# Performance work log

Measured on AMD Instinct MI355X. Metric: run time of the kernel, lower is better.

Reference implementation:

```python
import jax, jax.numpy as jnp
import numpy as np

NUM_CLASSES = 100
QUEUE_SIZE = 256
FEATURE_DIM = 1024
BATCH = 4096
EPS = 1e-12  # torch F.normalize eps


def _l2norm(x):
    n = jnp.linalg.norm(x, axis=-1, keepdims=True)
    return x / jnp.maximum(n, EPS)


def setup_inputs() -> dict:
    key = jax.random.key(0)
    k1, k2, k3, k4 = jax.random.split(key, 4)
    embeddings = jax.random.normal(k1, (BATCH, FEATURE_DIM), dtype=jnp.float32)
    labels = jax.random.randint(k2, (BATCH,), 0, NUM_CLASSES, dtype=jnp.int64)
    # buffer initialized as randn then L2-normalized (as in __init__)
    queue = _l2norm(jax.random.normal(k3, (NUM_CLASSES, QUEUE_SIZE, FEATURE_DIM), dtype=jnp.float32))
    queue_ptr = jax.random.randint(k4, (NUM_CLASSES,), 0, QUEUE_SIZE, dtype=jnp.int64)
    return {"embeddings": embeddings, "labels": labels, "queue": queue, "queue_ptr": queue_ptr}


def reference(embeddings, labels, queue, queue_ptr):
    # MemoryBank.update with tail_classes=None: store_idx == label.
    # Serial FIFO semantics: the k-th occurrence of class c in the batch is
    # written at slot (queue_ptr[c] + k) % queue_size.
    queue_size = queue.shape[1]
    emb = _l2norm(embeddings.astype(jnp.float32))  # (B, d)
    # rank[b] = number of earlier batch elements with the same label
    same = labels[:, None] == labels[None, :]           # (B, B)
    rank = jnp.sum(jnp.tril(same, k=-1), axis=1)        # (B,)
    slots = (queue_ptr[labels] + rank) % queue_size      # (B,)
    new_queue = queue.at[labels, slots].set(emb)
    return new_queue
```

## Files before the change

### kernel.cpp

```cpp
#include <hip/hip_runtime.h>

#define NUM_CLASSES 100
#define QUEUE_SIZE  256
#define FEATURE_DIM 1024
#define BATCH       4096
#define TOTAL_ROWS  (NUM_CLASSES * QUEUE_SIZE)
#define EPS         1e-12f

typedef float f32x4 __attribute__((ext_vector_type(4)));

__global__ __launch_bounds__(256) void compute_slots_kernel(
    const int* __restrict__ labels,
    const int* __restrict__ queue_ptr,
    int* __restrict__ inv)
{
    __shared__ int hist[NUM_CLASSES];
    __shared__ int s_lab[256];

    const int tid = threadIdx.x;
    const int chunk_start = blockIdx.x * 256;

    for (int i = tid; i < NUM_CLASSES; i += 256) hist[i] = 0;
    __syncthreads();

    for (int j = tid; j < chunk_start; j += 256) {
        atomicAdd(&hist[labels[j]], 1);
    }
    s_lab[tid] = labels[chunk_start + tid];
    __syncthreads();

    const int lab = s_lab[tid];
    int rank = hist[lab];
    for (int j = 0; j < tid; ++j) {
        rank += (s_lab[j] == lab) ? 1 : 0;
    }
    const int slot = (queue_ptr[lab] + rank) & (QUEUE_SIZE - 1);
    const int row  = lab * QUEUE_SIZE + slot;
    const int b    = chunk_start + tid;
    atomicMax(&inv[row], b);
}

__global__ __launch_bounds__(256) void fused_write_kernel(
    const float* __restrict__ queue,
    const float* __restrict__ emb,
    const int* __restrict__ inv,
    float* __restrict__ out)
{
    const int row = blockIdx.x;
    const int tid = threadIdx.x;
    const long base = (long)row * FEATURE_DIM;

    const int b = inv[row];

    if (b < 0) {
        const f32x4* src = reinterpret_cast<const f32x4*>(queue + base);
        f32x4*       dst = reinterpret_cast<f32x4*>(out + base);
        f32x4 v = __builtin_nontemporal_load(&src[tid]);
        __builtin_nontemporal_store(v, &dst[tid]);
        return;
    }

    const f32x4* src = reinterpret_cast<const f32x4*>(emb + (long)b * FEATURE_DIM);
    f32x4 v = src[tid];

    float ss = v.x * v.x + v.y * v.y + v.z * v.z + v.w * v.w;
    #pragma unroll
    for (int off = 32; off > 0; off >>= 1) {
        ss += __shfl_down(ss, off, 64);
    }

    __shared__ float s_part[4];
    const int lane = tid & 63;
    const int wave = tid >> 6;
    if (lane == 0) s_part[wave] = ss;
    __syncthreads();

    const float total = s_part[0] + s_part[1] + s_part[2] + s_part[3];
    const float inv_n = 1.0f / fmaxf(sqrtf(total), EPS);

    f32x4 o = v * inv_n;

    f32x4* dst = reinterpret_cast<f32x4*>(out + base);
    __builtin_nontemporal_store(o, &dst[tid]);
}

extern "C" void kernel_launch(void* const* d_in, const int* in_sizes, int n_in,
                              void* d_out, int out_size, void* d_ws, size_t ws_size,
                              hipStream_t stream)
{
    const float* embeddings = (const float*)d_in[0];
    const int*   labels     = (const int*)d_in[1];
    const float* queue      = (const float*)d_in[2];
    const int*   queue_ptr  = (const int*)d_in[3];

    float* out = (float*)d_out;
    int*   inv = (int*)d_ws;

    (void)hipMemsetAsync(inv, 0xFF, TOTAL_ROWS * sizeof(int), stream);

    compute_slots_kernel<<<BATCH / 256, 256, 0, stream>>>(labels, queue_ptr, inv);

    fused_write_kernel<<<TOTAL_ROWS, 256, 0, stream>>>(queue, embeddings, inv, out);
}
```

Measured before the change: 47.73 us.

## Compute slot inverse map per class with ballot compaction, drop memset and atomics

The slot computation is restructured so that each block owns one class. It scans all labels with wave ballots to build an ordered list of batch indices for that class, then directly computes which batch element, if any, lands in each of the 256 slots, keeping the last writer on wraparound. This removes the memset launch, the global atomicMax scatter and the O(chunk) prefix histogram per block. The trade-off is that each of the 100 blocks reads the full 4096 labels and uses 16KB of shared memory.

```diff
diff --git a/kernel.cpp b/kernel.cpp
--- a/kernel.cpp
+++ b/kernel.cpp
@@ -9,35 +9,54 @@
 
 typedef float f32x4 __attribute__((ext_vector_type(4)));
 
-__global__ __launch_bounds__(256) void compute_slots_kernel(
+__global__ __launch_bounds__(256) void slots_direct_kernel(
     const int* __restrict__ labels,
     const int* __restrict__ queue_ptr,
     int* __restrict__ inv)
 {
-    __shared__ int hist[NUM_CLASSES];
-    __shared__ int s_lab[256];
+    __shared__ int occ[BATCH];
+    __shared__ int wcnt[4];
 
-    const int tid = threadIdx.x;
-    const int chunk_start = blockIdx.x * 256;
+    const int c    = blockIdx.x;
+    const int tid  = threadIdx.x;
+    const int lane = tid & 63;
+    const int wave = tid >> 6;
+    const unsigned long long lt = (1ULL << lane) - 1ULL;
 
-    for (int i = tid; i < NUM_CLASSES; i += 256) hist[i] = 0;
+    int cnt_w = 0;
+    #pragma unroll 4
+    for (int i = 0; i < 16; ++i) {
+        const int b = wave * 1024 + i * 64 + lane;
+        const unsigned long long mask = __ballot(labels[b] == c);
+        cnt_w += __popcll(mask);
+    }
+    if (lane == 0) wcnt[wave] = cnt_w;
     __syncthreads();
 
-    for (int j = tid; j < chunk_start; j += 256) {
-        atomicAdd(&hist[labels[j]], 1);
+    int off = 0;
+    #pragma unroll
+    for (int w = 0; w < 4; ++w) off += (w < wave) ? wcnt[w] : 0;
+    const int cnt = wcnt[0] + wcnt[1] + wcnt[2] + wcnt[3];
+
+    #pragma unroll 4
+    for (int i = 0; i < 16; ++i) {
+        const int b = wave * 1024 + i * 64 + lane;
+        const bool m = (labels[b] == c);
+        const unsigned long long mask = __ballot(m);
+        if (m) occ[off + __popcll(mask & lt)] = b;
+        off += __popcll(mask);
     }
-    s_lab[tid] = labels[chunk_start + tid];
     __syncthreads();
 
-    const int lab = s_lab[tid];
-    int rank = hist[lab];
-    for (int j = 0; j < tid; ++j) {
-        rank += (s_lab[j] == lab) ? 1 : 0;
+    const int p  = queue_ptr[c] & (QUEUE_SIZE - 1);
+    const int s  = tid;
+    const int k0 = (s - p) & (QUEUE_SIZE - 1);
+    int b = -1;
+    if (k0 < cnt) {
+        const int k = k0 + (((cnt - 1 - k0) >> 8) << 8);
+        b = occ[k];
     }
-    const int slot = (queue_ptr[lab] + rank) & (QUEUE_SIZE - 1);
-    const int row  = lab * QUEUE_SIZE + slot;
-    const int b    = chunk_start + tid;
-    atomicMax(&inv[row], b);
+    inv[c * QUEUE_SIZE + s] = b;
 }
 
 __global__ __launch_bounds__(256) void fused_write_kernel(
@@ -96,9 +115,7 @@
     float* out = (float*)d_out;
     int*   inv = (int*)d_ws;
 
-    (void)hipMemsetAsync(inv, 0xFF, TOTAL_ROWS * sizeof(int), stream);
-
-    compute_slots_kernel<<<BATCH / 256, 256, 0, stream>>>(labels, queue_ptr, inv);
+    slots_direct_kernel<<<NUM_CLASSES, 256, 0, stream>>>(labels, queue_ptr, inv);
 
     fused_write_kernel<<<TOTAL_ROWS, 256, 0, stream>>>(queue, embeddings, inv, out);
 }
```

Result: faster. 40.98 us (-14.1%).
